# Performance work log

Measured on AMD Instinct MI355X. Metric: run time of the kernel, lower is better.

## Reference

```python
import jax, jax.numpy as jnp
import numpy as np

N = 65536   # total goals in library
D = 256     # flattened embedding dim
B = 2048    # batch_size (last B entries are the new batch)


def setup_inputs() -> dict:
    key = jax.random.key(0)
    k1, k2 = jax.random.split(key)
    return {
        "target_lib": jax.random.normal(k1, (N, D), dtype=jnp.float32),
        "reached_lib": jax.random.normal(k2, (N, D), dtype=jnp.float32),
        "batch_size": B,
    }


def _euclid(a, b):
    # distance_fn: Euclidean distance between two embeddings
    return jnp.sqrt(jnp.sum((a - b) ** 2))


def _nearest_idx(queries, lib):
    # top-1 nearest neighbor via squared-distance expansion (same argmin as cdist)
    qn = jnp.sum(queries * queries, axis=1, keepdims=True)      # [B,1]
    ln = jnp.sum(lib * lib, axis=1)                             # [L]
    d2 = qn + ln[None, :] - 2.0 * (queries @ lib.T)             # [B,L]
    return jnp.argmin(d2, axis=1)                               # [B]


def reference(target_lib, reached_lib, batch_size):
    targets = target_lib[-batch_size:]          # [B,D] newest target goals
    reached = reached_lib[-batch_size:]         # [B,D] newest reached goals
    prev = reached_lib[:-batch_size]            # [N-B,D] previously reached goals

    prev_closest = prev[_nearest_idx(targets, prev)]       # [B,D]
    new_closest = reached[_nearest_idx(targets, reached)]  # [B,D]

    def LP(t, init_e, reached_e):
        return _euclid(t, init_e) - _euclid(t, reached_e)

    IM_vals, IM_grads = jax.vmap(jax.value_and_grad(LP, 0))(
        targets, prev_closest, new_closest)
    return IM_vals, IM_grads
```

## Files before the change

### kernel.cpp

```cpp
#include <hip/hip_runtime.h>
#include <math.h>

#define NTOT   65536
#define DDIM   256
#define BATCH  2048
#define NPREV  (NTOT - BATCH)

#define NC_P 31
#define CHUNK_P 2048
#define NC_R 16
#define CHUNK_R 128

#define INF_F 3.402823466e+38f
#define SWZ(r) ((((r) & 3)) ^ ((((r) >> 2) & 3)))

typedef float  f32x4 __attribute__((ext_vector_type(4)));
typedef _Float16 half8 __attribute__((ext_vector_type(8)));

#define TILE_HALVES 65536
#define KB_HALVES   8192

__global__ void lp_norms(const float* __restrict__ lib, float* __restrict__ ln) {
    const int row  = blockIdx.x * 4 + (threadIdx.x >> 6);
    const int lane = threadIdx.x & 63;
    const float4 v = reinterpret_cast<const float4*>(lib + (size_t)row * DDIM)[lane];
    float s = v.x * v.x + v.y * v.y + v.z * v.z + v.w * v.w;
#pragma unroll
    for (int off = 32; off > 0; off >>= 1) s += __shfl_down(s, off);
    if (lane == 0) ln[row] = s;
}

__device__ __forceinline__ void cvt_split(const f32x4 a, const f32x4 b,
                                          half8& h, half8& l) {
    float v[8] = {a[0], a[1], a[2], a[3], b[0], b[1], b[2], b[3]};
#pragma unroll
    for (int j = 0; j < 8; ++j) {
        const float s = v[j] * 256.0f;
        const _Float16 hh = (_Float16)s;
        const _Float16 ll = (_Float16)(s - (float)hh);
        h[j] = hh; l[j] = ll;
    }
}

__global__ void lp_split(const float* __restrict__ src, _Float16* __restrict__ dst,
                         float* __restrict__ ln) {
    const int tile = blockIdx.x;
    const int t    = threadIdx.x;
    const int rlo  = t >> 2;
    const int s    = t & 3;
    const float* srcT = src + (size_t)tile * 128 * DDIM;
    _Float16*    dstT = dst + (size_t)tile * TILE_HALVES;

    float n0 = 0.f, n1 = 0.f;
#pragma unroll
    for (int kb = 0; kb < 8; ++kb) {
#pragma unroll
        for (int sub = 0; sub < 2; ++sub) {
            const int r  = rlo + 64 * sub;
            const int ks = s ^ SWZ(r);
            const float* p = srcT + (size_t)r * DDIM + kb * 32 + ks * 8;
            const f32x4 a = *reinterpret_cast<const f32x4*>(p);
            const f32x4 b = *reinterpret_cast<const f32x4*>(p + 4);
            half8 h, l; cvt_split(a, b, h, l);
            _Float16* base = dstT + kb * KB_HALVES + (r * 4 + s) * 8;
            *reinterpret_cast<half8*>(base)        = h;
            *reinterpret_cast<half8*>(base + 4096) = l;
            const float ss = a[0]*a[0] + a[1]*a[1] + a[2]*a[2] + a[3]*a[3]
                           + b[0]*b[0] + b[1]*b[1] + b[2]*b[2] + b[3]*b[3];
            if (sub == 0) n0 += ss; else n1 += ss;
        }
    }
    if (ln != nullptr) {
        n0 += __shfl_xor(n0, 1); n0 += __shfl_xor(n0, 2);
        n1 += __shfl_xor(n1, 1); n1 += __shfl_xor(n1, 2);
        if (s == 0) {
            ln[(size_t)tile * 128 + rlo]      = n0;
            ln[(size_t)tile * 128 + rlo + 64] = n1;
        }
    }
}

__device__ __forceinline__ void stage4k(_Float16* lds, const _Float16* g, int t) {
    const int wid = t >> 6;
    __builtin_amdgcn_global_load_lds(
        (const __attribute__((address_space(1))) void*)(g + (size_t)t * 8),
        (__attribute__((address_space(3))) void*)(lds + (size_t)wid * 512),
        16, 0, 0);
}

__global__ __launch_bounds__(256, 2)
void lp_nn_mfma3(const _Float16* __restrict__ Qs, const _Float16* __restrict__ Ls,
                 const float* __restrict__ ln, int chunkRows,
                 float* __restrict__ pscore, int* __restrict__ pidx, int nchunks)
{
    __shared__ _Float16 B0[4][4096];
    __shared__ _Float16 B1[4][4096];
    __shared__ float xk[2][128];
    __shared__ int   xi[2][128];

    const int nwg  = 16 * nchunks;
    const int hid  = blockIdx.x;
    const int work = (hid & 7) * (nwg >> 3) + (hid >> 3);
    const int bx   = work & 15;
    const int by   = work >> 4;

    const int t    = threadIdx.x;
    const int wid  = t >> 6, lane = t & 63;
    const int wq   = wid >> 1, wl = wid & 1;
    const int col  = lane & 15, rg = lane >> 4;
    const int chunkBase = by * chunkRows;

    const _Float16* Qtile = Qs + (size_t)bx * TILE_HALVES;
    const _Float16* Lbase = Ls + (size_t)(chunkBase >> 7) * TILE_HALVES;
    const int NSTEP = (chunkRows >> 7) * 8;

    float bkey[4][4];
    int   bidxr[4][4];
    f32x4 acc[4][4];
#pragma unroll
    for (int mf = 0; mf < 4; ++mf)
#pragma unroll
        for (int i = 0; i < 4; ++i) {
            bkey[mf][i] = INF_F; bidxr[mf][i] = 0x7fffffff;
            acc[mf][i] = (f32x4)(0.f);
        }

    auto stage = [&](_Float16 (&dst)[4][4096], int s) {
        const int kb = s & 7, lt = s >> 3;
        const _Float16* Qkb = Qtile + kb * KB_HALVES;
        const _Float16* Lkb = Lbase + (size_t)lt * TILE_HALVES + kb * KB_HALVES;
        stage4k(&dst[0][0],    Qkb,        t);
        stage4k(&dst[0][2048], Qkb + 2048, t);
        stage4k(&dst[1][0],    Qkb + 4096, t);
        stage4k(&dst[1][2048], Qkb + 6144, t);
        stage4k(&dst[2][0],    Lkb,        t);
        stage4k(&dst[2][2048], Lkb + 2048, t);
        stage4k(&dst[3][0],    Lkb + 4096, t);
        stage4k(&dst[3][2048], Lkb + 6144, t);
    };

    auto compute = [&](const _Float16 (&buf)[4][4096], int s) {
        half8 ah[4], al[4];
#pragma unroll
        for (int mf = 0; mf < 4; ++mf) {
            const int r = wq * 64 + mf * 16 + col;
            const int sw = rg ^ SWZ(r);
            ah[mf] = *reinterpret_cast<const half8*>(&buf[0][r * 32 + sw * 8]);
            al[mf] = *reinterpret_cast<const half8*>(&buf[1][r * 32 + sw * 8]);
        }
#pragma unroll
        for (int nf = 0; nf < 4; ++nf) {
            const int r = wl * 64 + nf * 16 + col;
            const int sw = rg ^ SWZ(r);
            const half8 bh = *reinterpret_cast<const half8*>(&buf[2][r * 32 + sw * 8]);
            const half8 bl = *reinterpret_cast<const half8*>(&buf[3][r * 32 + sw * 8]);
#pragma unroll
            for (int mf = 0; mf < 4; ++mf) {
                acc[mf][nf] = __builtin_amdgcn_mfma_f32_16x16x32_f16(ah[mf], bh, acc[mf][nf], 0, 0, 0);
                acc[mf][nf] = __builtin_amdgcn_mfma_f32_16x16x32_f16(ah[mf], bl, acc[mf][nf], 0, 0, 0);
                acc[mf][nf] = __builtin_amdgcn_mfma_f32_16x16x32_f16(al[mf], bh, acc[mf][nf], 0, 0, 0);
            }
        }
        if ((s & 7) == 7) {
            const int ltbase = chunkBase + ((s >> 3) << 7);
#pragma unroll
            for (int nf = 0; nf < 4; ++nf) {
                const int gidx = ltbase + wl * 64 + nf * 16 + col;
                const float lnv = ln[gidx] * 65536.0f;
#pragma unroll
                for (int mf = 0; mf < 4; ++mf)
#pragma unroll
                    for (int i = 0; i < 4; ++i) {
                        const float key = fmaf(-2.f, acc[mf][nf][i], lnv);
                        if (key < bkey[mf][i] || (key == bkey[mf][i] && gidx < bidxr[mf][i])) {
                            bkey[mf][i] = key; bidxr[mf][i] = gidx;
                        }
                        acc[mf][nf][i] = 0.f;
                    }
            }
        }
    };

    stage(B0, 0);
    __syncthreads();
    for (int s = 0; s < NSTEP; s += 2) {
        stage(B1, s + 1);
        compute(B0, s);
        __syncthreads();
        if (s + 2 < NSTEP) stage(B0, s + 2);
        compute(B1, s + 1);
        __syncthreads();
    }

#pragma unroll
    for (int off = 1; off < 16; off <<= 1) {
#pragma unroll
        for (int mf = 0; mf < 4; ++mf)
#pragma unroll
            for (int i = 0; i < 4; ++i) {
                const float ok = __shfl_xor(bkey[mf][i], off);
                const int   oi = __shfl_xor(bidxr[mf][i], off);
                if (ok < bkey[mf][i] || (ok == bkey[mf][i] && oi < bidxr[mf][i])) {
                    bkey[mf][i] = ok; bidxr[mf][i] = oi;
                }
            }
    }
    if (col == 0) {
#pragma unroll
        for (int mf = 0; mf < 4; ++mf)
#pragma unroll
            for (int i = 0; i < 4; ++i) {
                const int ql = wq * 64 + mf * 16 + rg * 4 + i;
                xk[wl][ql] = bkey[mf][i];
                xi[wl][ql] = bidxr[mf][i];
            }
    }
    __syncthreads();
    if (t < 128) {
        float bk = xk[0][t]; int bi = xi[0][t];
        const float k2 = xk[1][t]; const int i2 = xi[1][t];
        if (k2 < bk || (k2 == bk && i2 < bi)) { bk = k2; bi = i2; }
        const int q = bx * 128 + t;
        pscore[(size_t)q * nchunks + by] = bk;
        pidx  [(size_t)q * nchunks + by] = bi;
    }
}

__global__ __launch_bounds__(256, 2)
void lp_nn_mfma_fb(const float* __restrict__ Q, const float* __restrict__ L,
                   const float* __restrict__ ln, int chunkRows,
                   float* __restrict__ pscore, int* __restrict__ pidx, int nchunks)
{
    __shared__ _Float16 Ah[128 * 32];
    __shared__ _Float16 Al[128 * 32];
    __shared__ _Float16 Bh[128 * 32];
    __shared__ _Float16 Bl[128 * 32];
    __shared__ float xk[2][128];
    __shared__ int   xi[2][128];

    const int t    = threadIdx.x;
    const int wid  = t >> 6, lane = t & 63;
    const int wq   = wid >> 1, wl = wid & 1;
    const int col  = lane & 15, rg = lane >> 4;
    const int qbase = blockIdx.x * 128;
    const int chunkBase = blockIdx.y * chunkRows;
    const int srow   = t >> 2;
    const int schunk = t & 3;

    float bkey[4][4];
    int   bidxr[4][4];
#pragma unroll
    for (int mf = 0; mf < 4; ++mf)
#pragma unroll
        for (int i = 0; i < 4; ++i) { bkey[mf][i] = INF_F; bidxr[mf][i] = 0x7fffffff; }

    for (int lt = 0; lt < chunkRows; lt += 128) {
        f32x4 acc[4][4];
#pragma unroll
        for (int mf = 0; mf < 4; ++mf)
#pragma unroll
            for (int nf = 0; nf < 4; ++nf) acc[mf][nf] = (f32x4)(0.f);

        for (int kb = 0; kb < DDIM; kb += 32) {
            __syncthreads();
#pragma unroll
            for (int sr = 0; sr < 2; ++sr) {
                const int r = srow + 64 * sr;
                const int s = schunk ^ SWZ(r);
                {
                    const float* src = Q + (size_t)(qbase + r) * DDIM + kb + schunk * 8;
                    const f32x4 a = *reinterpret_cast<const f32x4*>(src);
                    const f32x4 b = *reinterpret_cast<const f32x4*>(src + 4);
                    half8 h, l; cvt_split(a, b, h, l);
                    *reinterpret_cast<half8*>(&Ah[r * 32 + s * 8]) = h;
                    *reinterpret_cast<half8*>(&Al[r * 32 + s * 8]) = l;
                }
                {
                    const float* src = L + (size_t)(chunkBase + lt + r) * DDIM + kb + schunk * 8;
                    const f32x4 a = *reinterpret_cast<const f32x4*>(src);
                    const f32x4 b = *reinterpret_cast<const f32x4*>(src + 4);
                    half8 h, l; cvt_split(a, b, h, l);
                    *reinterpret_cast<half8*>(&Bh[r * 32 + s * 8]) = h;
                    *reinterpret_cast<half8*>(&Bl[r * 32 + s * 8]) = l;
                }
            }
            __syncthreads();

            half8 ah[4], al[4];
#pragma unroll
            for (int mf = 0; mf < 4; ++mf) {
                const int r = wq * 64 + mf * 16 + col;
                const int s = rg ^ SWZ(r);
                ah[mf] = *reinterpret_cast<const half8*>(&Ah[r * 32 + s * 8]);
                al[mf] = *reinterpret_cast<const half8*>(&Al[r * 32 + s * 8]);
            }
#pragma unroll
            for (int nf = 0; nf < 4; ++nf) {
                const int r = wl * 64 + nf * 16 + col;
                const int s = rg ^ SWZ(r);
                const half8 bh = *reinterpret_cast<const half8*>(&Bh[r * 32 + s * 8]);
                const half8 bl = *reinterpret_cast<const half8*>(&Bl[r * 32 + s * 8]);
#pragma unroll
                for (int mf = 0; mf < 4; ++mf) {
                    acc[mf][nf] = __builtin_amdgcn_mfma_f32_16x16x32_f16(ah[mf], bh, acc[mf][nf], 0, 0, 0);
                    acc[mf][nf] = __builtin_amdgcn_mfma_f32_16x16x32_f16(ah[mf], bl, acc[mf][nf], 0, 0, 0);
                    acc[mf][nf] = __builtin_amdgcn_mfma_f32_16x16x32_f16(al[mf], bh, acc[mf][nf], 0, 0, 0);
                }
            }
        }

#pragma unroll
        for (int nf = 0; nf < 4; ++nf) {
            const int gidx = chunkBase + lt + wl * 64 + nf * 16 + col;
            const float lnv = ln[gidx] * 65536.0f;
#pragma unroll
            for (int mf = 0; mf < 4; ++mf)
#pragma unroll
                for (int i = 0; i < 4; ++i) {
                    const float key = fmaf(-2.f, acc[mf][nf][i], lnv);
                    if (key < bkey[mf][i] || (key == bkey[mf][i] && gidx < bidxr[mf][i])) {
                        bkey[mf][i] = key; bidxr[mf][i] = gidx;
                    }
                }
        }
    }

#pragma unroll
    for (int off = 1; off < 16; off <<= 1) {
#pragma unroll
        for (int mf = 0; mf < 4; ++mf)
#pragma unroll
            for (int i = 0; i < 4; ++i) {
                const float ok = __shfl_xor(bkey[mf][i], off);
                const int   oi = __shfl_xor(bidxr[mf][i], off);
                if (ok < bkey[mf][i] || (ok == bkey[mf][i] && oi < bidxr[mf][i])) {
                    bkey[mf][i] = ok; bidxr[mf][i] = oi;
                }
            }
    }
    if (col == 0) {
#pragma unroll
        for (int mf = 0; mf < 4; ++mf)
#pragma unroll
            for (int i = 0; i < 4; ++i) {
                const int ql = wq * 64 + mf * 16 + rg * 4 + i;
                xk[wl][ql] = bkey[mf][i];
                xi[wl][ql] = bidxr[mf][i];
            }
    }
    __syncthreads();
    if (t < 128) {
        float bk = xk[0][t]; int bi = xi[0][t];
        const float k2 = xk[1][t]; const int i2 = xi[1][t];
        if (k2 < bk || (k2 == bk && i2 < bi)) { bk = k2; bi = i2; }
        const int q = qbase + t;
        pscore[(size_t)q * nchunks + blockIdx.y] = bk;
        pidx  [(size_t)q * nchunks + blockIdx.y] = bi;
    }
}

__global__ void lp_finalize(const float* __restrict__ Q,
                            const float* __restrict__ prevL,
                            const float* __restrict__ reachL,
                            const float* __restrict__ ps_p, const int* __restrict__ pi_p,
                            const float* __restrict__ ps_r, const int* __restrict__ pi_r,
                            float* __restrict__ out)
{
    const int q = blockIdx.x;
    const int lane = threadIdx.x;

    float k1 = (lane < NC_P) ? ps_p[(size_t)q * NC_P + lane] : INF_F;
    int   i1 = (lane < NC_P) ? pi_p[(size_t)q * NC_P + lane] : 0x7fffffff;
#pragma unroll
    for (int off = 32; off > 0; off >>= 1) {
        const float ok = __shfl_xor(k1, off);
        const int   oi = __shfl_xor(i1, off);
        if (ok < k1 || (ok == k1 && oi < i1)) { k1 = ok; i1 = oi; }
    }
    float k2 = (lane < NC_R) ? ps_r[(size_t)q * NC_R + lane] : INF_F;
    int   i2 = (lane < NC_R) ? pi_r[(size_t)q * NC_R + lane] : 0x7fffffff;
#pragma unroll
    for (int off = 32; off > 0; off >>= 1) {
        const float ok = __shfl_xor(k2, off);
        const int   oi = __shfl_xor(i2, off);
        if (ok < k2 || (ok == k2 && oi < i2)) { k2 = ok; i2 = oi; }
    }

    const float4 tv = reinterpret_cast<const float4*>(Q      + (size_t)q  * DDIM)[lane];
    const float4 e1 = reinterpret_cast<const float4*>(prevL  + (size_t)i1 * DDIM)[lane];
    const float4 e2 = reinterpret_cast<const float4*>(reachL + (size_t)i2 * DDIM)[lane];
    const float4 d1 = {tv.x - e1.x, tv.y - e1.y, tv.z - e1.z, tv.w - e1.w};
    const float4 d2 = {tv.x - e2.x, tv.y - e2.y, tv.z - e2.z, tv.w - e2.w};
    float s1 = d1.x * d1.x + d1.y * d1.y + d1.z * d1.z + d1.w * d1.w;
    float s2 = d2.x * d2.x + d2.y * d2.y + d2.z * d2.z + d2.w * d2.w;
#pragma unroll
    for (int off = 32; off > 0; off >>= 1) {
        s1 += __shfl_xor(s1, off);
        s2 += __shfl_xor(s2, off);
    }
    const float r1 = sqrtf(s1), r2 = sqrtf(s2);
    float4 g;
    g.x = d1.x / r1 - d2.x / r2;
    g.y = d1.y / r1 - d2.y / r2;
    g.z = d1.z / r1 - d2.z / r2;
    g.w = d1.w / r1 - d2.w / r2;
    reinterpret_cast<float4*>(out + BATCH + (size_t)q * DDIM)[lane] = g;
    if (lane == 0) out[q] = r1 - r2;
}

extern "C" void kernel_launch(void* const* d_in, const int* in_sizes, int n_in,
                              void* d_out, int out_size, void* d_ws, size_t ws_size,
                              hipStream_t stream) {
    const float* target_lib  = (const float*)d_in[0];
    const float* reached_lib = (const float*)d_in[1];
    const float* Qp     = target_lib  + (size_t)NPREV * DDIM;
    const float* prevL  = reached_lib;
    const float* reachL = reached_lib + (size_t)NPREV * DDIM;

    float* ws     = (float*)d_ws;
    float* ln_all = ws;
    float* ps_p   = ln_all + NTOT;
    float* ps_r   = ps_p + (size_t)BATCH * NC_P;
    int*   pi_p   = (int*)(ps_r + (size_t)BATCH * NC_R);
    int*   pi_r   = pi_p + (size_t)BATCH * NC_P;
    _Float16* Qsp = (_Float16*)(pi_r + (size_t)BATCH * NC_R);
    _Float16* Lsp = Qsp + (size_t)(BATCH / 128) * TILE_HALVES;
    float* out    = (float*)d_out;

    const size_t need = 1032192u
                      + (size_t)(BATCH / 128) * TILE_HALVES * 2
                      + (size_t)(NTOT / 128) * TILE_HALVES * 2;

    if (ws_size >= need) {
        lp_split<<<NTOT / 128, 256, 0, stream>>>(reached_lib, Lsp, ln_all);
        lp_split<<<BATCH / 128, 256, 0, stream>>>(Qp, Qsp, nullptr);
        lp_nn_mfma3<<<16 * NC_P, 256, 0, stream>>>(
            Qsp, Lsp, ln_all, CHUNK_P, ps_p, pi_p, NC_P);
        lp_nn_mfma3<<<16 * NC_R, 256, 0, stream>>>(
            Qsp, Lsp + (size_t)(NPREV / 128) * TILE_HALVES,
            ln_all + NPREV, CHUNK_R, ps_r, pi_r, NC_R);
    } else {
        lp_norms<<<NTOT / 4, 256, 0, stream>>>(reached_lib, ln_all);
        lp_nn_mfma_fb<<<dim3(BATCH / 128, NC_P), 256, 0, stream>>>(
            Qp, prevL, ln_all, CHUNK_P, ps_p, pi_p, NC_P);
        lp_nn_mfma_fb<<<dim3(BATCH / 128, NC_R), 256, 0, stream>>>(
            Qp, reachL, ln_all + NPREV, CHUNK_R, ps_r, pi_r, NC_R);
    }
    lp_finalize<<<BATCH, 64, 0, stream>>>(Qp, prevL, reachL, ps_p, pi_p, ps_r, pi_r, out);
}
```

Baseline: 262.2 us.

## Switch nearest-neighbor GEMM to 32x32x16 MFMA with fragment-native split layout

Replaces the 16x16x32 MFMA tiling with 32x32x16 MFMA instructions, each wave computing 2x2 32x32 fragments. The split kernel now writes the fp16 hi/lo data directly in per-lane fragment order, so LDS reads become linear half8 loads with no swizzle. The intent is fewer MFMA issues and fewer LDS fragment loads per FLOP. In exchange, the argmin epilogue and the cross-lane reduction over 16-element accumulators now use more registers and more shuffles.

```diff
diff --git a/kernel.cpp b/kernel.cpp
--- a/kernel.cpp
+++ b/kernel.cpp
@@ -14,7 +14,8 @@
 #define INF_F 3.402823466e+38f
 #define SWZ(r) ((((r) & 3)) ^ ((((r) >> 2) & 3)))
 
-typedef float  f32x4 __attribute__((ext_vector_type(4)));
+typedef float  f32x4  __attribute__((ext_vector_type(4)));
+typedef float  f32x16 __attribute__((ext_vector_type(16)));
 typedef _Float16 half8 __attribute__((ext_vector_type(8)));
 
 #define TILE_HALVES 65536
@@ -42,42 +43,35 @@
     }
 }
 
-__global__ void lp_split(const float* __restrict__ src, _Float16* __restrict__ dst,
-                         float* __restrict__ ln) {
+__global__ void lp_split32(const float* __restrict__ src, _Float16* __restrict__ dst,
+                           float* __restrict__ ln) {
     const int tile = blockIdx.x;
     const int t    = threadIdx.x;
-    const int rlo  = t >> 2;
-    const int s    = t & 3;
-    const float* srcT = src + (size_t)tile * 128 * DDIM;
+    const int rg   = t >> 6;
+    const int l    = t & 63;
+    const int row  = rg * 32 + (l & 31);
+    const int k8   = l >> 5;
+    const float* srcR = src + (size_t)tile * 128 * DDIM + (size_t)row * DDIM;
     _Float16*    dstT = dst + (size_t)tile * TILE_HALVES;
 
-    float n0 = 0.f, n1 = 0.f;
+    float nsum = 0.f;
 #pragma unroll
     for (int kb = 0; kb < 8; ++kb) {
 #pragma unroll
-        for (int sub = 0; sub < 2; ++sub) {
-            const int r  = rlo + 64 * sub;
-            const int ks = s ^ SWZ(r);
-            const float* p = srcT + (size_t)r * DDIM + kb * 32 + ks * 8;
+        for (int kk = 0; kk < 2; ++kk) {
+            const float* p = srcR + kb * 32 + kk * 16 + k8 * 8;
             const f32x4 a = *reinterpret_cast<const f32x4*>(p);
             const f32x4 b = *reinterpret_cast<const f32x4*>(p + 4);
-            half8 h, l; cvt_split(a, b, h, l);
-            _Float16* base = dstT + kb * KB_HALVES + (r * 4 + s) * 8;
-            *reinterpret_cast<half8*>(base)        = h;
-            *reinterpret_cast<half8*>(base + 4096) = l;
-            const float ss = a[0]*a[0] + a[1]*a[1] + a[2]*a[2] + a[3]*a[3]
-                           + b[0]*b[0] + b[1]*b[1] + b[2]*b[2] + b[3]*b[3];
-            if (sub == 0) n0 += ss; else n1 += ss;
+            half8 h, lo; cvt_split(a, b, h, lo);
+            const size_t off = ((size_t)(((kb * 2 + 0) * 4 + rg) * 2 + kk) * 64 + l) * 8;
+            *reinterpret_cast<half8*>(dstT + off)        = h;
+            *reinterpret_cast<half8*>(dstT + off + 4096) = lo;
+            nsum += a[0]*a[0] + a[1]*a[1] + a[2]*a[2] + a[3]*a[3]
+                  + b[0]*b[0] + b[1]*b[1] + b[2]*b[2] + b[3]*b[3];
         }
     }
-    if (ln != nullptr) {
-        n0 += __shfl_xor(n0, 1); n0 += __shfl_xor(n0, 2);
-        n1 += __shfl_xor(n1, 1); n1 += __shfl_xor(n1, 2);
-        if (s == 0) {
-            ln[(size_t)tile * 128 + rlo]      = n0;
-            ln[(size_t)tile * 128 + rlo + 64] = n1;
-        }
-    }
+    nsum += __shfl_xor(nsum, 32);
+    if (ln != nullptr && k8 == 0) ln[(size_t)tile * 128 + row] = nsum;
 }
 
 __device__ __forceinline__ void stage4k(_Float16* lds, const _Float16* g, int t) {
@@ -89,12 +83,12 @@
 }
 
 __global__ __launch_bounds__(256, 2)
-void lp_nn_mfma3(const _Float16* __restrict__ Qs, const _Float16* __restrict__ Ls,
+void lp_nn_mfma4(const _Float16* __restrict__ Qs, const _Float16* __restrict__ Ls,
                  const float* __restrict__ ln, int chunkRows,
                  float* __restrict__ pscore, int* __restrict__ pidx, int nchunks)
 {
-    __shared__ _Float16 B0[4][4096];
-    __shared__ _Float16 B1[4][4096];
+    __shared__ _Float16 B0[16384];
+    __shared__ _Float16 B1[16384];
     __shared__ float xk[2][128];
     __shared__ int   xi[2][128];
 
@@ -107,75 +101,73 @@
     const int t    = threadIdx.x;
     const int wid  = t >> 6, lane = t & 63;
     const int wq   = wid >> 1, wl = wid & 1;
-    const int col  = lane & 15, rg = lane >> 4;
+    const int col  = lane & 31, hi = lane >> 5;
     const int chunkBase = by * chunkRows;
 
     const _Float16* Qtile = Qs + (size_t)bx * TILE_HALVES;
     const _Float16* Lbase = Ls + (size_t)(chunkBase >> 7) * TILE_HALVES;
     const int NSTEP = (chunkRows >> 7) * 8;
 
-    float bkey[4][4];
-    int   bidxr[4][4];
-    f32x4 acc[4][4];
-#pragma unroll
-    for (int mf = 0; mf < 4; ++mf)
-#pragma unroll
-        for (int i = 0; i < 4; ++i) {
-            bkey[mf][i] = INF_F; bidxr[mf][i] = 0x7fffffff;
-            acc[mf][i] = (f32x4)(0.f);
-        }
-
-    auto stage = [&](_Float16 (&dst)[4][4096], int s) {
+    float bkey[2][16];
+    int   bidxr[2][16];
+    f32x16 acc[2][2];
+#pragma unroll
+    for (int mf = 0; mf < 2; ++mf) {
+#pragma unroll
+        for (int r = 0; r < 16; ++r) { bkey[mf][r] = INF_F; bidxr[mf][r] = 0x7fffffff; }
+#pragma unroll
+        for (int nf = 0; nf < 2; ++nf) acc[mf][nf] = (f32x16)(0.f);
+    }
+
+    auto stage = [&](_Float16* dst, int s) {
         const int kb = s & 7, lt = s >> 3;
         const _Float16* Qkb = Qtile + kb * KB_HALVES;
         const _Float16* Lkb = Lbase + (size_t)lt * TILE_HALVES + kb * KB_HALVES;
-        stage4k(&dst[0][0],    Qkb,        t);
-        stage4k(&dst[0][2048], Qkb + 2048, t);
-        stage4k(&dst[1][0],    Qkb + 4096, t);
-        stage4k(&dst[1][2048], Qkb + 6144, t);
-        stage4k(&dst[2][0],    Lkb,        t);
-        stage4k(&dst[2][2048], Lkb + 2048, t);
-        stage4k(&dst[3][0],    Lkb + 4096, t);
-        stage4k(&dst[3][2048], Lkb + 6144, t);
+#pragma unroll
+        for (int i = 0; i < 4; ++i) stage4k(dst + i * 2048,        Qkb + i * 2048, t);
+#pragma unroll
+        for (int i = 0; i < 4; ++i) stage4k(dst + 8192 + i * 2048, Lkb + i * 2048, t);
     };
 
-    auto compute = [&](const _Float16 (&buf)[4][4096], int s) {
-        half8 ah[4], al[4];
-#pragma unroll
-        for (int mf = 0; mf < 4; ++mf) {
-            const int r = wq * 64 + mf * 16 + col;
-            const int sw = rg ^ SWZ(r);
-            ah[mf] = *reinterpret_cast<const half8*>(&buf[0][r * 32 + sw * 8]);
-            al[mf] = *reinterpret_cast<const half8*>(&buf[1][r * 32 + sw * 8]);
-        }
-#pragma unroll
-        for (int nf = 0; nf < 4; ++nf) {
-            const int r = wl * 64 + nf * 16 + col;
-            const int sw = rg ^ SWZ(r);
-            const half8 bh = *reinterpret_cast<const half8*>(&buf[2][r * 32 + sw * 8]);
-            const half8 bl = *reinterpret_cast<const half8*>(&buf[3][r * 32 + sw * 8]);
-#pragma unroll
-            for (int mf = 0; mf < 4; ++mf) {
-                acc[mf][nf] = __builtin_amdgcn_mfma_f32_16x16x32_f16(ah[mf], bh, acc[mf][nf], 0, 0, 0);
-                acc[mf][nf] = __builtin_amdgcn_mfma_f32_16x16x32_f16(ah[mf], bl, acc[mf][nf], 0, 0, 0);
-                acc[mf][nf] = __builtin_amdgcn_mfma_f32_16x16x32_f16(al[mf], bh, acc[mf][nf], 0, 0, 0);
-            }
+    auto compute = [&](const _Float16* buf, int s) {
+        const _Float16* Ab = buf;
+        const _Float16* Bb = buf + 8192;
+#pragma unroll
+        for (int kk = 0; kk < 2; ++kk) {
+            half8 a[2][2], b[2][2];
+#pragma unroll
+            for (int mf = 0; mf < 2; ++mf)
+#pragma unroll
+                for (int hl = 0; hl < 2; ++hl) {
+                    a[mf][hl] = *reinterpret_cast<const half8*>(
+                        Ab + (((hl * 4 + (wq * 2 + mf)) * 2 + kk) * 64 + lane) * 8);
+                    b[mf][hl] = *reinterpret_cast<const half8*>(
+                        Bb + (((hl * 4 + (wl * 2 + mf)) * 2 + kk) * 64 + lane) * 8);
+                }
+#pragma unroll
+            for (int nf = 0; nf < 2; ++nf)
+#pragma unroll
+                for (int mf = 0; mf < 2; ++mf) {
+                    acc[mf][nf] = __builtin_amdgcn_mfma_f32_32x32x16_f16(a[mf][0], b[nf][0], acc[mf][nf], 0, 0, 0);
+                    acc[mf][nf] = __builtin_amdgcn_mfma_f32_32x32x16_f16(a[mf][0], b[nf][1], acc[mf][nf], 0, 0, 0);
+                    acc[mf][nf] = __builtin_amdgcn_mfma_f32_32x32x16_f16(a[mf][1], b[nf][0], acc[mf][nf], 0, 0, 0);
+                }
         }
         if ((s & 7) == 7) {
             const int ltbase = chunkBase + ((s >> 3) << 7);
 #pragma unroll
-            for (int nf = 0; nf < 4; ++nf) {
-                const int gidx = ltbase + wl * 64 + nf * 16 + col;
+            for (int nf = 0; nf < 2; ++nf) {
+                const int gidx = ltbase + wl * 64 + nf * 32 + col;
                 const float lnv = ln[gidx] * 65536.0f;
 #pragma unroll
-                for (int mf = 0; mf < 4; ++mf)
-#pragma unroll
-                    for (int i = 0; i < 4; ++i) {
-                        const float key = fmaf(-2.f, acc[mf][nf][i], lnv);
-                        if (key < bkey[mf][i] || (key == bkey[mf][i] && gidx < bidxr[mf][i])) {
-                            bkey[mf][i] = key; bidxr[mf][i] = gidx;
+                for (int mf = 0; mf < 2; ++mf)
+#pragma unroll
+                    for (int r = 0; r < 16; ++r) {
+                        const float key = fmaf(-2.f, acc[mf][nf][r], lnv);
+                        if (key < bkey[mf][r] || (key == bkey[mf][r] && gidx < bidxr[mf][r])) {
+                            bkey[mf][r] = key; bidxr[mf][r] = gidx;
                         }
-                        acc[mf][nf][i] = 0.f;
+                        acc[mf][nf][r] = 0.f;
                     }
             }
         }
@@ -193,26 +185,26 @@
     }
 
 #pragma unroll
-    for (int off = 1; off < 16; off <<= 1) {
-#pragma unroll
-        for (int mf = 0; mf < 4; ++mf)
-#pragma unroll
-            for (int i = 0; i < 4; ++i) {
-                const float ok = __shfl_xor(bkey[mf][i], off);
-                const int   oi = __shfl_xor(bidxr[mf][i], off);
-                if (ok < bkey[mf][i] || (ok == bkey[mf][i] && oi < bidxr[mf][i])) {
-                    bkey[mf][i] = ok; bidxr[mf][i] = oi;
+    for (int off = 1; off < 32; off <<= 1) {
+#pragma unroll
+        for (int mf = 0; mf < 2; ++mf)
+#pragma unroll
+            for (int r = 0; r < 16; ++r) {
+                const float ok = __shfl_xor(bkey[mf][r], off);
+                const int   oi = __shfl_xor(bidxr[mf][r], off);
+                if (ok < bkey[mf][r] || (ok == bkey[mf][r] && oi < bidxr[mf][r])) {
+                    bkey[mf][r] = ok; bidxr[mf][r] = oi;
                 }
             }
     }
     if (col == 0) {
 #pragma unroll
-        for (int mf = 0; mf < 4; ++mf)
-#pragma unroll
-            for (int i = 0; i < 4; ++i) {
-                const int ql = wq * 64 + mf * 16 + rg * 4 + i;
-                xk[wl][ql] = bkey[mf][i];
-                xi[wl][ql] = bidxr[mf][i];
+        for (int mf = 0; mf < 2; ++mf)
+#pragma unroll
+            for (int r = 0; r < 16; ++r) {
+                const int ql = wq * 64 + mf * 32 + (r & 3) + 8 * (r >> 2) + 4 * hi;
+                xk[wl][ql] = bkey[mf][r];
+                xi[wl][ql] = bidxr[mf][r];
             }
     }
     __syncthreads();
@@ -432,11 +424,11 @@
                       + (size_t)(NTOT / 128) * TILE_HALVES * 2;
 
     if (ws_size >= need) {
-        lp_split<<<NTOT / 128, 256, 0, stream>>>(reached_lib, Lsp, ln_all);
-        lp_split<<<BATCH / 128, 256, 0, stream>>>(Qp, Qsp, nullptr);
-        lp_nn_mfma3<<<16 * NC_P, 256, 0, stream>>>(
+        lp_split32<<<NTOT / 128, 256, 0, stream>>>(reached_lib, Lsp, ln_all);
+        lp_split32<<<BATCH / 128, 256, 0, stream>>>(Qp, Qsp, nullptr);
+        lp_nn_mfma4<<<16 * NC_P, 256, 0, stream>>>(
             Qsp, Lsp, ln_all, CHUNK_P, ps_p, pi_p, NC_P);
-        lp_nn_mfma3<<<16 * NC_R, 256, 0, stream>>>(
+        lp_nn_mfma4<<<16 * NC_R, 256, 0, stream>>>(
             Qsp, Lsp + (size_t)(NPREV / 128) * TILE_HALVES,
             ln_all + NPREV, CHUNK_R, ps_r, pi_r, NC_R);
     } else {
```

Result: slower. 282.2 us (+7.6%).
